# Kernel tuning notes

Hardware: AMD Instinct MI355X
Metric: run time of the kernel (lower is better)

The kernel has to match this reference:

```python
import jax, jax.numpy as jnp
import numpy as np

NQ = 5  # 1 ancilla qubit (index 0) + 4 register qubits (indices 1..4)


def setup_inputs():
    key = jax.random.key(0)
    k1, k2 = jax.random.split(key)
    inputs = jax.random.uniform(k1, (32, 32, 32, 3), dtype=jnp.float32)
    kernel = jax.random.normal(k2, (8, 1, 15), dtype=jnp.float32) * 0.3
    return {"inputs": inputs, "kernel": kernel}


def _apply1(state, U, q):
    # state: [P, 2,2,2,2,2]; U: [2,2] or [P,2,2]; qubit q at axis q+1
    state = jnp.moveaxis(state, q + 1, -1)
    if U.ndim == 3:
        state = jnp.einsum('nij,n...j->n...i', U, state)
    else:
        state = jnp.einsum('ij,n...j->n...i', U, state)
    return jnp.moveaxis(state, -1, q + 1)


def _apply2(state, U, qa, qb):
    # U: [4,4] acting on (qa, qb)
    state = jnp.moveaxis(state, (qa + 1, qb + 1), (-2, -1))
    sh = state.shape
    state = state.reshape(sh[:-2] + (4,))
    state = jnp.einsum('ij,n...j->n...i', U, state)
    state = state.reshape(sh)
    return jnp.moveaxis(state, (-2, -1), (qa + 1, qb + 1))


def _rx_batch(theta):
    # cirq.rx(theta): [[cos(t/2), -i sin(t/2)], [-i sin(t/2), cos(t/2)]]; theta: [P]
    c = jnp.cos(theta / 2).astype(jnp.complex64)
    s = jnp.sin(theta / 2).astype(jnp.complex64)
    return jnp.stack([jnp.stack([c, -1j * s], -1), jnp.stack([-1j * s, c], -1)], -2)


def _cxpow(e):
    # CXPowGate(exponent=e): identity on control=0 block, X^e on control=1 block
    o = jnp.ones((), jnp.complex64)
    z = jnp.zeros((), jnp.complex64)
    lam = jnp.exp(1j * jnp.pi * e.astype(jnp.complex64))
    a = (o + lam) / 2
    b = (o - lam) / 2
    return jnp.stack([jnp.stack([o, z, z, z]), jnp.stack([z, o, z, z]),
                      jnp.stack([z, z, a, b]), jnp.stack([z, z, b, a])])


def _czpow(e):
    o = jnp.ones((), jnp.complex64)
    lam = jnp.exp(1j * jnp.pi * e.astype(jnp.complex64))
    return jnp.diag(jnp.stack([o, o, o, lam]))


def _simulate(angles, params):
    # angles: [P, 4*C] pixel values per patch; params: [5*C] learned exponents
    P = angles.shape[0]
    C = angles.shape[1] // 4
    state = jnp.zeros((P, 2 ** NQ), jnp.complex64).at[:, 0].set(1.0)
    state = state.reshape((P,) + (2,) * NQ)
    Hm = jnp.asarray(np.array([[1, 1], [1, -1]]) / np.sqrt(2), jnp.complex64)
    state = _apply1(state, Hm, 0)  # H on ancilla
    for j in range(C):
        # embed: rx(pi * pixel) on the 4 register qubits
        for i in range(4):
            state = _apply1(state, _rx_batch(jnp.pi * angles[:, 4 * j + i]), 1 + i)
        p = params[5 * j:5 * j + 5]
        # intra-register entanglement: CXPow with (control, target) pairs
        for g, (qc, qt) in enumerate(((1, 2), (2, 3), (3, 4), (4, 1))):
            state = _apply2(state, _cxpow(p[g]), qc, qt)
        # deposit: CZPow between register qubit 0 and the ancilla (symmetric)
        state = _apply2(state, _czpow(p[4]), 1, 0)
    # <X_0> = 2 Re sum conj(psi[0,rest]) psi[1,rest]
    exp = 2.0 * jnp.sum(jnp.real(jnp.conj(state[:, 0]) * state[:, 1]),
                        axis=tuple(range(1, NQ)))
    return exp.astype(jnp.float32)  # [P]


def reference(inputs, kernel):
    B, H, W, C = inputs.shape
    nx, ny = H - 1, W - 1
    # normalize_tensor_by_index: inputs already in [0,1] -> identity
    x = inputs
    # 2x2 stride-1 patches; last axis order (0,0),(0,1),(1,0),(1,1) row-major
    p = jnp.stack([x[:, :-1, :-1], x[:, :-1, 1:], x[:, 1:, :-1], x[:, 1:, 1:]], axis=-1)
    # [B,nx,ny,C,4] -> [B*nx*ny, C*4]: index 4*c + pixel (channel-major, matches transpose+reshape in call())
    angles = p.reshape(-1, C * 4)
    params = kernel[:, 0, :]  # [K, 5*C]
    exp = jax.vmap(lambda pr: _simulate(angles, pr))(params)  # [K, B*nx*ny]
    out = exp.reshape(params.shape[0], B, nx, ny).transpose(1, 2, 3, 0)  # [B,nx,ny,K]
    out = jnp.arccos(jnp.clip(out, -1 + 1e-5, 1 - 1e-5)) / jnp.pi
    return out  # activation=None -> linear
```

## Files before the change

kernel.cpp:

```cpp
#include <hip/hip_runtime.h>
#include <math.h>

#define PI_F 3.14159265358979323846f


template<int S>
__device__ __forceinline__ void rx16(float* sr, float* si, float c, float s) {
#pragma unroll
    for (int i = 0; i < 16; ++i) {
        if (i & S) continue;
        const int j = i + S;
        const float r0 = sr[i], m0 = si[i], r1 = sr[j], m1 = si[j];
        sr[i] = fmaf(c, r0,  s * m1);
        si[i] = fmaf(c, m0, -s * r1);
        sr[j] = fmaf(c, r1,  s * m0);
        si[j] = fmaf(c, m1, -s * r0);
    }
}

template<int Sc, int St>
__device__ __forceinline__ void cx16(float* sr, float* si, float br, float bi) {
#pragma unroll
    for (int i = 0; i < 16; ++i) {
        if (!(i & Sc) || (i & St)) continue;
        const int j = i + St;
        const float dr = sr[j] - sr[i], di = si[j] - si[i];
        const float ur = br * dr - bi * di;
        const float ui = fmaf(br, di, bi * dr);
        sr[i] += ur; si[i] += ui;
        sr[j] -= ur; si[j] -= ui;
    }
}

__device__ __forceinline__ void cz16(float* sr, float* si, float cl, float sl) {
#pragma unroll
    for (int m = 0; m < 16; ++m) {
        if (!(m & 8)) continue;
        const float r = sr[m], q = si[m];
        sr[m] = r * cl - q * sl;
        si[m] = fmaf(r, sl, q * cl);
    }
}

__device__ __forceinline__ void bcoef(float e, float& br, float& bi) {
    const float rev = e * 0.5f;
    const float sl = __builtin_amdgcn_sinf(rev);
    const float cl = __builtin_amdgcn_cosf(rev);
    br = 0.5f * (1.0f - cl);
    bi = -0.5f * sl;
}

__global__ __launch_bounds__(256)
void u1_circuit_kernel(const float* __restrict__ inp,
                       const float* __restrict__ ker,
                       float* __restrict__ out,
                       int total) {
    const int t = blockIdx.x * blockDim.x + threadIdx.x;
    if (t >= total) return;

    const int r   = t & 7;
    const int pix = t >> 3;
    const int iy  = pix % 31;
    const int tq  = pix / 31;
    const int ix  = tq % 31;
    const int b   = tq / 31;

    const float* xp = inp + ((size_t)(b * 32 + ix) * 32 + iy) * 3;
    const float* pp = ker + r * 15;

    float c1, s1, c2, s2, c3, s3, c4, s4;
    {
        const float a0 = xp[0], a1 = xp[3], a2 = xp[96], a3 = xp[99];
        s1 = __builtin_amdgcn_sinf(a0 * 0.25f); c1 = __builtin_amdgcn_cosf(a0 * 0.25f);
        s2 = __builtin_amdgcn_sinf(a1 * 0.25f); c2 = __builtin_amdgcn_cosf(a1 * 0.25f);
        s3 = __builtin_amdgcn_sinf(a2 * 0.25f); c3 = __builtin_amdgcn_cosf(a2 * 0.25f);
        s4 = __builtin_amdgcn_sinf(a3 * 0.25f); c4 = __builtin_amdgcn_cosf(a3 * 0.25f);
    }
    float t2[4], t3[8], mg[16];
    t2[0] = c1 * c2; t2[1] = c1 * s2; t2[2] = s1 * c2; t2[3] = s1 * s2;
#pragma unroll
    for (int x = 0; x < 8; ++x)  t3[x] = t2[x >> 1] * ((x & 1) ? s3 : c3);
#pragma unroll
    for (int x = 0; x < 16; ++x) mg[x] = t3[x >> 1] * ((x & 1) ? s4 : c4);

    float p0r[16], p0i[16];
#pragma unroll
    for (int m = 0; m < 16; ++m) {
        const int pc = __builtin_popcount(m) & 3;
        p0r[m] = (pc == 0) ? mg[m] : ((pc == 2) ? -mg[m] : 0.0f);
        p0i[m] = (pc == 1) ? -mg[m] : ((pc == 3) ? mg[m] : 0.0f);
    }

    float br, bi;
    bcoef(pp[0], br, bi); cx16<8, 4>(p0r, p0i, br, bi);
    bcoef(pp[1], br, bi); cx16<4, 2>(p0r, p0i, br, bi);
    bcoef(pp[2], br, bi); cx16<2, 1>(p0r, p0i, br, bi);
    bcoef(pp[3], br, bi); cx16<1, 8>(p0r, p0i, br, bi);

    float p1r[16], p1i[16];
    {
        const float rev = pp[4] * 0.5f;
        const float sl = __builtin_amdgcn_sinf(rev);
        const float cl = __builtin_amdgcn_cosf(rev);
#pragma unroll
        for (int m = 0; m < 16; ++m) {
            if (m & 8) {
                p1r[m] = p0r[m] * cl - p0i[m] * sl;
                p1i[m] = fmaf(p0r[m], sl, p0i[m] * cl);
            } else {
                p1r[m] = p0r[m];
                p1i[m] = p0i[m];
            }
        }
    }

#pragma unroll
    for (int j = 1; j < 3; ++j) {
        const float a0 = xp[j], a1 = xp[3 + j], a2 = xp[96 + j], a3 = xp[99 + j];
        float c, s;
        s = __builtin_amdgcn_sinf(a0 * 0.25f); c = __builtin_amdgcn_cosf(a0 * 0.25f);
        rx16<8>(p0r, p0i, c, s); rx16<8>(p1r, p1i, c, s);
        s = __builtin_amdgcn_sinf(a1 * 0.25f); c = __builtin_amdgcn_cosf(a1 * 0.25f);
        rx16<4>(p0r, p0i, c, s); rx16<4>(p1r, p1i, c, s);
        s = __builtin_amdgcn_sinf(a2 * 0.25f); c = __builtin_amdgcn_cosf(a2 * 0.25f);
        rx16<2>(p0r, p0i, c, s); rx16<2>(p1r, p1i, c, s);
        s = __builtin_amdgcn_sinf(a3 * 0.25f); c = __builtin_amdgcn_cosf(a3 * 0.25f);
        rx16<1>(p0r, p0i, c, s); rx16<1>(p1r, p1i, c, s);

        const float* p = pp + 5 * j;
        bcoef(p[0], br, bi); cx16<8, 4>(p0r, p0i, br, bi); cx16<8, 4>(p1r, p1i, br, bi);
        bcoef(p[1], br, bi); cx16<4, 2>(p0r, p0i, br, bi); cx16<4, 2>(p1r, p1i, br, bi);
        bcoef(p[2], br, bi); cx16<2, 1>(p0r, p0i, br, bi); cx16<2, 1>(p1r, p1i, br, bi);
        bcoef(p[3], br, bi); cx16<1, 8>(p0r, p0i, br, bi); cx16<1, 8>(p1r, p1i, br, bi);

        const float rev = p[4] * 0.5f;
        cz16(p1r, p1i, __builtin_amdgcn_cosf(rev), __builtin_amdgcn_sinf(rev));
    }

    float dot = 0.0f;
#pragma unroll
    for (int m = 0; m < 16; ++m)
        dot = fmaf(p0r[m], p1r[m], fmaf(p0i[m], p1i[m], dot));

    dot = fminf(fmaxf(dot, -1.0f + 1e-5f), 1.0f - 1e-5f);
    out[t] = acosf(dot) * (1.0f / PI_F);
}

extern "C" void kernel_launch(void* const* d_in, const int* in_sizes, int n_in,
                              void* d_out, int out_size, void* d_ws, size_t ws_size,
                              hipStream_t stream) {
    const float* inp = (const float*)d_in[0];
    const float* ker = (const float*)d_in[1];
    float* out = (float*)d_out;
    const int total = out_size;
    const int block = 256;
    const int grid = (total + block - 1) / block;
    u1_circuit_kernel<<<grid, block, 0, stream>>>(inp, ker, out, total);
}
```

Baseline: 67.43 us.

## Split each circuit's two ancilla branches across paired threads and use polynomial acos

Each simulation now runs on two adjacent threads, one per ancilla branch (with or without the controlled phase), instead of one thread tracking both 16-amplitude branches. The final overlap is combined with cross-lane shuffles. This halves per-thread register state and arithmetic to raise occupancy and parallelism, at the cost of duplicated input loads, trig and shared gate work across the pair. The library acosf is also replaced with a short polynomial approximation (Abramowitz-Stegun style), which lowers accuracy slightly.

```diff
diff --git a/kernel.cpp b/kernel.cpp
--- a/kernel.cpp
+++ b/kernel.cpp
@@ -51,15 +51,17 @@
 }
 
 __global__ __launch_bounds__(256)
-void u1_circuit_kernel(const float* __restrict__ inp,
-                       const float* __restrict__ ker,
-                       float* __restrict__ out,
-                       int total) {
-    const int t = blockIdx.x * blockDim.x + threadIdx.x;
-    if (t >= total) return;
+void u1_split_kernel(const float* __restrict__ inp,
+                     const float* __restrict__ ker,
+                     float* __restrict__ out,
+                     int nsim) {
+    const int t   = blockIdx.x * blockDim.x + threadIdx.x;
+    const int sim = t >> 1;
+    if (sim >= nsim) return;
+    const int h   = t & 1;
 
-    const int r   = t & 7;
-    const int pix = t >> 3;
+    const int r   = sim & 7;
+    const int pix = sim >> 3;
     const int iy  = pix % 31;
     const int tq  = pix / 31;
     const int ix  = tq % 31;
@@ -83,35 +85,24 @@
 #pragma unroll
     for (int x = 0; x < 16; ++x) mg[x] = t3[x >> 1] * ((x & 1) ? s4 : c4);
 
-    float p0r[16], p0i[16];
+    float sr[16], si[16];
 #pragma unroll
     for (int m = 0; m < 16; ++m) {
         const int pc = __builtin_popcount(m) & 3;
-        p0r[m] = (pc == 0) ? mg[m] : ((pc == 2) ? -mg[m] : 0.0f);
-        p0i[m] = (pc == 1) ? -mg[m] : ((pc == 3) ? mg[m] : 0.0f);
+        sr[m] = (pc == 0) ? mg[m] : ((pc == 2) ? -mg[m] : 0.0f);
+        si[m] = (pc == 1) ? -mg[m] : ((pc == 3) ? mg[m] : 0.0f);
     }
 
     float br, bi;
-    bcoef(pp[0], br, bi); cx16<8, 4>(p0r, p0i, br, bi);
-    bcoef(pp[1], br, bi); cx16<4, 2>(p0r, p0i, br, bi);
-    bcoef(pp[2], br, bi); cx16<2, 1>(p0r, p0i, br, bi);
-    bcoef(pp[3], br, bi); cx16<1, 8>(p0r, p0i, br, bi);
-
-    float p1r[16], p1i[16];
+    bcoef(pp[0], br, bi); cx16<8, 4>(sr, si, br, bi);
+    bcoef(pp[1], br, bi); cx16<4, 2>(sr, si, br, bi);
+    bcoef(pp[2], br, bi); cx16<2, 1>(sr, si, br, bi);
+    bcoef(pp[3], br, bi); cx16<1, 8>(sr, si, br, bi);
     {
         const float rev = pp[4] * 0.5f;
         const float sl = __builtin_amdgcn_sinf(rev);
         const float cl = __builtin_amdgcn_cosf(rev);
-#pragma unroll
-        for (int m = 0; m < 16; ++m) {
-            if (m & 8) {
-                p1r[m] = p0r[m] * cl - p0i[m] * sl;
-                p1i[m] = fmaf(p0r[m], sl, p0i[m] * cl);
-            } else {
-                p1r[m] = p0r[m];
-                p1i[m] = p0i[m];
-            }
-        }
+        cz16(sr, si, h ? cl : 1.0f, h ? sl : 0.0f);
     }
 
 #pragma unroll
@@ -119,31 +110,44 @@
         const float a0 = xp[j], a1 = xp[3 + j], a2 = xp[96 + j], a3 = xp[99 + j];
         float c, s;
         s = __builtin_amdgcn_sinf(a0 * 0.25f); c = __builtin_amdgcn_cosf(a0 * 0.25f);
-        rx16<8>(p0r, p0i, c, s); rx16<8>(p1r, p1i, c, s);
+        rx16<8>(sr, si, c, s);
         s = __builtin_amdgcn_sinf(a1 * 0.25f); c = __builtin_amdgcn_cosf(a1 * 0.25f);
-        rx16<4>(p0r, p0i, c, s); rx16<4>(p1r, p1i, c, s);
+        rx16<4>(sr, si, c, s);
         s = __builtin_amdgcn_sinf(a2 * 0.25f); c = __builtin_amdgcn_cosf(a2 * 0.25f);
-        rx16<2>(p0r, p0i, c, s); rx16<2>(p1r, p1i, c, s);
+        rx16<2>(sr, si, c, s);
         s = __builtin_amdgcn_sinf(a3 * 0.25f); c = __builtin_amdgcn_cosf(a3 * 0.25f);
-        rx16<1>(p0r, p0i, c, s); rx16<1>(p1r, p1i, c, s);
+        rx16<1>(sr, si, c, s);
 
         const float* p = pp + 5 * j;
-        bcoef(p[0], br, bi); cx16<8, 4>(p0r, p0i, br, bi); cx16<8, 4>(p1r, p1i, br, bi);
-        bcoef(p[1], br, bi); cx16<4, 2>(p0r, p0i, br, bi); cx16<4, 2>(p1r, p1i, br, bi);
-        bcoef(p[2], br, bi); cx16<2, 1>(p0r, p0i, br, bi); cx16<2, 1>(p1r, p1i, br, bi);
-        bcoef(p[3], br, bi); cx16<1, 8>(p0r, p0i, br, bi); cx16<1, 8>(p1r, p1i, br, bi);
+        bcoef(p[0], br, bi); cx16<8, 4>(sr, si, br, bi);
+        bcoef(p[1], br, bi); cx16<4, 2>(sr, si, br, bi);
+        bcoef(p[2], br, bi); cx16<2, 1>(sr, si, br, bi);
+        bcoef(p[3], br, bi); cx16<1, 8>(sr, si, br, bi);
 
         const float rev = p[4] * 0.5f;
-        cz16(p1r, p1i, __builtin_amdgcn_cosf(rev), __builtin_amdgcn_sinf(rev));
+        const float sl = __builtin_amdgcn_sinf(rev);
+        const float cl = __builtin_amdgcn_cosf(rev);
+        cz16(sr, si, h ? cl : 1.0f, h ? sl : 0.0f);
     }
 
     float dot = 0.0f;
 #pragma unroll
-    for (int m = 0; m < 16; ++m)
-        dot = fmaf(p0r[m], p1r[m], fmaf(p0i[m], p1i[m], dot));
+    for (int m = 0; m < 16; ++m) {
+        const float orr = __shfl_xor(sr[m], 1);
+        const float oii = __shfl_xor(si[m], 1);
+        dot = fmaf(sr[m], orr, fmaf(si[m], oii, dot));
+    }
 
-    dot = fminf(fmaxf(dot, -1.0f + 1e-5f), 1.0f - 1e-5f);
-    out[t] = acosf(dot) * (1.0f / PI_F);
+    float x = fminf(fmaxf(dot, -1.0f + 1e-5f), 1.0f - 1e-5f);
+    const float a  = fabsf(x);
+    const float sq = __builtin_amdgcn_sqrtf(1.0f - a);
+    float pl = fmaf(a, -0.0187293f, 0.0742610f);
+    pl = fmaf(a, pl, -0.2121144f);
+    pl = fmaf(a, pl, 1.5707288f);
+    float ac = sq * pl;
+    if (x < 0.0f) ac = PI_F - ac;
+
+    if (h == 0) out[sim] = ac * (1.0f / PI_F);
 }
 
 extern "C" void kernel_launch(void* const* d_in, const int* in_sizes, int n_in,
@@ -152,8 +156,9 @@
     const float* inp = (const float*)d_in[0];
     const float* ker = (const float*)d_in[1];
     float* out = (float*)d_out;
-    const int total = out_size;
+    const int nsim = out_size;
+    const int total = nsim * 2;
     const int block = 256;
     const int grid = (total + block - 1) / block;
-    u1_circuit_kernel<<<grid, block, 0, stream>>>(inp, ker, out, total);
+    u1_split_kernel<<<grid, block, 0, stream>>>(inp, ker, out, nsim);
 }
```

After: 72.59 us. 1.08x slower.
